# Kernel optimization log

Hardware: AMD Instinct MI355X
Metric: run time of the kernel (lower is better)

Reference implementation:

```python
import jax, jax.numpy as jnp
import numpy as np

ALPHA = 0.2        # LeakyReLU negative slope (config['alpha'])
NEG_INF = -9e15    # mask value from the original code


def setup_inputs() -> dict:
    key = jax.random.key(0)
    k1, k2, k3, k4 = jax.random.split(key, 4)
    N, Fin, Fout = 8192, 512, 256
    inp = jax.random.normal(k1, (N, Fin), dtype=jnp.float32)
    adj = jax.random.randint(k2, (N, N), 0, 2, dtype=jnp.int32)
    # xavier_uniform with gain=1.414
    limW = 1.414 * np.sqrt(6.0 / (Fin + Fout))
    W = jax.random.uniform(k3, (Fin, Fout), dtype=jnp.float32, minval=-limW, maxval=limW)
    lima = 1.414 * np.sqrt(6.0 / (2 * Fout + 1))
    a = jax.random.uniform(k4, (2 * Fout, 1), dtype=jnp.float32, minval=-lima, maxval=lima)
    return {"input": inp, "adj": adj, "W": W, "a": a}


def reference(input, adj, W, a):
    # h: [N, F]
    h = input @ W
    Fout = W.shape[1]
    # The original builds a_input[i, j] = concat(h_i, h_j) and dots with a.
    # Equivalently: e_ij = leakyrelu(h_i . a[:F] + h_j . a[F:]), computed
    # without the O(N^2 * 2F) intermediate.
    s1 = h @ a[:Fout, 0]   # [N] contribution from node i
    s2 = h @ a[Fout:, 0]   # [N] contribution from node j
    e = s1[:, None] + s2[None, :]                     # [N, N]
    e = jnp.where(e > 0, e, ALPHA * e)                # LeakyReLU
    scores = jnp.where(adj > 0, e, NEG_INF)
    attention = jax.nn.softmax(scores, axis=1)        # row-wise softmax
    # dropout is identity in inference mode (training=False)
    h_prime = attention @ h                           # [N, F]
    return jax.nn.elu(h_prime)                        # concat=True path
```

## Files before the change

### kernel.cpp

```cpp
#include <hip/hip_runtime.h>
#include <stdint.h>
#include <stddef.h>


#define N_NODES 8192
#define FIN     512
#define FOUT    256
#define LRALPHA 0.2f
#define MI_SHIFT 16.0f

typedef float f32x4 __attribute__((ext_vector_type(4)));
typedef short s16x8 __attribute__((ext_vector_type(8)));
typedef unsigned short u16x4 __attribute__((ext_vector_type(4)));
typedef int   i32x4 __attribute__((ext_vector_type(4)));
typedef unsigned long long u64;

typedef const uint32_t __attribute__((address_space(1)))* gas1_u32;
typedef uint32_t __attribute__((address_space(3)))* las3_u32;

__device__ __forceinline__ short f2bf_rne(float f) {
  uint32_t u = __builtin_bit_cast(uint32_t, f);
  u += 0x7fffu + ((u >> 16) & 1u);
  return (short)(u >> 16);
}
__device__ __forceinline__ short f2bf_fast(float f) {
  uint32_t u = __builtin_bit_cast(uint32_t, f);
  return (short)((u + 0x8000u) >> 16);
}
__device__ __forceinline__ float bf2f(short s) {
  uint32_t u = ((uint32_t)(uint16_t)s) << 16;
  return __builtin_bit_cast(float, u);
}

__global__ __launch_bounds__(256) void k_prep(const float* __restrict__ W,
                                              uint16_t* __restrict__ WThi,
                                              uint16_t* __restrict__ WTlo) {
  const int idx = blockIdx.x * 256 + threadIdx.x;
  const int n = idx >> 9;
  const int k = idx & 511;
  float v = W[k * FOUT + n];
  short h = f2bf_rne(v);
  WThi[idx] = (uint16_t)h;
  WTlo[idx] = (uint16_t)f2bf_rne(v - bf2f(h));
}

__global__ __launch_bounds__(256, 4) void k_pre(const float* __restrict__ X,
                                                const uint16_t* __restrict__ WThi,
                                                const uint16_t* __restrict__ WTlo,
                                                const float* __restrict__ a,
                                                const int* __restrict__ adj,
                                                uint16_t* __restrict__ HTf,
                                                float* __restrict__ s1g,
                                                float* __restrict__ s2g,
                                                u64* __restrict__ M3) {
  __shared__ float ls1[16], ls2[16];
  __shared__ uint16_t tile[FOUT * 16];
  const int lane = threadIdx.x & 63;
  const int w    = threadIdx.x >> 6;

  if (blockIdx.x >= 512) {
    const int bxm  = blockIdx.x - 512;
    const int iblk = bxm >> 5;
    const int jc   = bxm & 31;
    const int L    = lane;
    const int* base = adj + (size_t)(iblk * 128 + w * 32) * N_NODES + jc * 256 + L;
    u64 keep0 = 0, keep1 = 0, keep2 = 0, keep3 = 0;
#pragma unroll
    for (int it = 0; it < 32; ++it) {
      const int* rp = base + (size_t)it * N_NODES;
      int v0 = rp[0], v1 = rp[64], v2 = rp[128], v3 = rp[192];
      u64 b0 = __ballot(v0 != 0);
      u64 b1 = __ballot(v1 != 0);
      u64 b2 = __ballot(v2 != 0);
      u64 b3 = __ballot(v3 != 0);
      if (L == it) { keep0 = b0; keep1 = b1; keep2 = b2; keep3 = b3; }
    }
    if (L < 32) {
      const size_t mb = (size_t)iblk * 128 * 128 + (w * 32 + L);
      M3[mb + (size_t)(jc * 4 + 0) * 128] = keep0;
      M3[mb + (size_t)(jc * 4 + 1) * 128] = keep1;
      M3[mb + (size_t)(jc * 4 + 2) * 128] = keep2;
      M3[mb + (size_t)(jc * 4 + 3) * 128] = keep3;
    }
    return;
  }

  const int m    = lane & 15;
  const int quad = lane >> 4;
  const int i0   = blockIdx.x * 16;
  const int colg = w * 64;

  f32x4 acc[4];
#pragma unroll
  for (int cb = 0; cb < 4; ++cb) { f32x4 z = {0.f,0.f,0.f,0.f}; acc[cb] = z; }

  for (int kt = 0; kt < FIN / 32; ++kt) {
    const int k0 = kt * 32 + quad * 8;
    const float* ap = X + (size_t)(i0 + m) * FIN + k0;
    f32x4 a0 = *(const f32x4*)ap;
    f32x4 a1 = *(const f32x4*)(ap + 4);
    s16x8 ahi, alo;
#pragma unroll
    for (int e = 0; e < 4; ++e) {
      short h0 = f2bf_rne(a0[e]); ahi[e] = h0; alo[e] = f2bf_rne(a0[e] - bf2f(h0));
      short h1 = f2bf_rne(a1[e]); ahi[4+e] = h1; alo[4+e] = f2bf_rne(a1[e] - bf2f(h1));
    }
#pragma unroll
    for (int cb = 0; cb < 4; ++cb) {
      const int n = colg + cb * 16 + m;
      s16x8 bhi = *(const s16x8*)(WThi + (size_t)n * FIN + k0);
      s16x8 blo = *(const s16x8*)(WTlo + (size_t)n * FIN + k0);
      acc[cb] = __builtin_amdgcn_mfma_f32_16x16x32_bf16(ahi, bhi, acc[cb], 0, 0, 0);
      acc[cb] = __builtin_amdgcn_mfma_f32_16x16x32_bf16(ahi, blo, acc[cb], 0, 0, 0);
      acc[cb] = __builtin_amdgcn_mfma_f32_16x16x32_bf16(alo, bhi, acc[cb], 0, 0, 0);
    }
  }

  float p1[4] = {0.f,0.f,0.f,0.f}, p2[4] = {0.f,0.f,0.f,0.f};
#pragma unroll
  for (int cb = 0; cb < 4; ++cb) {
    const int n = colg + cb * 16 + m;
    const float a1c = a[n];
    const float a2c = a[FOUT + n];
#pragma unroll
    for (int reg = 0; reg < 4; ++reg) {
      p1[reg] += acc[cb][reg] * a1c;
      p2[reg] += acc[cb][reg] * a2c;
    }
  }
#pragma unroll
  for (int off = 1; off <= 8; off <<= 1)
#pragma unroll
    for (int reg = 0; reg < 4; ++reg) {
      p1[reg] += __shfl_xor(p1[reg], off);
      p2[reg] += __shfl_xor(p2[reg], off);
    }
  if (threadIdx.x < 16) { ls1[threadIdx.x] = 0.f; ls2[threadIdx.x] = 0.f; }
  __syncthreads();
  if (m == 0) {
#pragma unroll
    for (int reg = 0; reg < 4; ++reg) {
      atomicAdd(&ls1[quad * 4 + reg], p1[reg]);
      atomicAdd(&ls2[quad * 4 + reg], p2[reg]);
    }
  }
#pragma unroll
  for (int cb = 0; cb < 4; ++cb) {
    const int col = colg + cb * 16 + m;
    u16x4 pk;
#pragma unroll
    for (int reg = 0; reg < 4; ++reg) pk[reg] = (uint16_t)f2bf_rne(acc[cb][reg]);
    *(u16x4*)(tile + col * 16 + quad * 4) = pk;
  }
  __syncthreads();
  const int t = threadIdx.x;
  if (t < 16) { s1g[i0 + t] = ls1[t]; s2g[i0 + t] = ls2[t]; }
  const int jt = i0 >> 5;
  const int qh = (i0 >> 4) & 1;
  const int c  = t >> 4;
  const int mm = t & 15;
#pragma unroll
  for (int qq = 0; qq < 2; ++qq) {
    uint4 v = *(const uint4*)(tile + (c * 16 + mm) * 16 + qq * 8);
    *(uint4*)(HTf + ((((size_t)jt * 16 + c) * 64) + (qh * 2 + qq) * 16 + mm) * 8) = v;
  }
}

__global__ __launch_bounds__(512, 4) void k_attn(const u64* __restrict__ M3,
                                                 const uint16_t* __restrict__ HTf,
                                                 const float* __restrict__ s1,
                                                 const float* __restrict__ s2,
                                                 float* __restrict__ pout,
                                                 float* __restrict__ pden,
                                                 int split) {
  __shared__ uint16_t PL[2][4096];
  __shared__ uint16_t BL[2][8192];
  __shared__ float lss2[1024];
  __shared__ float ldsden[512];

  const int tid  = threadIdx.x;
  const int lane = tid & 63;
  const int w    = tid >> 6;
  const int m    = lane & 15;
  const int q    = lane >> 4;
  const int rg   = w >> 2, cg = w & 3;
  const int r    = tid & 127;
  const int cpr  = tid >> 7;
  const int i0   = blockIdx.x * 128;
  const int sp   = blockIdx.y;
  const int jrange = N_NODES / split;
  const int jbeg   = sp * jrange;
  const int jblk   = jbeg >> 5;
  const int nphase = jrange / 32;

  const float s1r = s1[i0 + r];
  float mi = fmaxf(s1r + MI_SHIFT, LRALPHA * (s1r + MI_SHIFT));

  f32x4 acc[4][4];
#pragma unroll
  for (int rt = 0; rt < 4; ++rt)
#pragma unroll
    for (int cb = 0; cb < 4; ++cb) { f32x4 z = {0.f,0.f,0.f,0.f}; acc[rt][cb] = z; }
  float den = 0.f;

  const u64* mrow = M3 + ((size_t)blockIdx.x * 128 + (jbeg >> 6)) * 128 + r;
  u64 mcur = mrow[0];

#define STAGE_B(pp, buf) do {                                                  \
    const uint16_t* s_ = HTf + (((size_t)(jblk + (pp))) << 13) + (w << 10) +   \
                         (lane << 3);                                          \
    __builtin_amdgcn_global_load_lds((gas1_u32)(const void*)s_,                \
        (las3_u32)(void*)(&BL[buf][w << 10]), 16, 0, 0);                       \
    __builtin_amdgcn_global_load_lds((gas1_u32)(const void*)(s_ + 512),        \
        (las3_u32)(void*)(&BL[buf][(w << 10) + 512]), 16, 0, 0);               \
  } while (0)

  STAGE_B(0, 0);

#pragma unroll 1
  for (int ph = 0; ph < nphase; ph += 2) {
    if ((ph & 31) == 0) {
      __syncthreads();
      if (tid < 256) *(f32x4*)(lss2 + tid * 4) =
        *(const f32x4*)(s2 + jbeg + (ph >> 5) * 1024 + tid * 4);
      __syncthreads();
    }
    u64 mnx = (ph + 2 < nphase) ? mrow[((ph >> 1) + 1) * 128] : 0;
#pragma unroll
    for (int po = 0; po < 2; ++po) {
      const int p = ph + po;
      const int pl = p & 31;
      f32x4 sA = *(const f32x4*)(lss2 + pl * 32 + cpr * 8);
      f32x4 sB = *(const f32x4*)(lss2 + pl * 32 + cpr * 8 + 4);
      const uint32_t by = (uint32_t)(mcur >> ((po * 4 + cpr) * 8)) & 0xffu;
      s16x8 P0;
#pragma unroll
      for (int e = 0; e < 4; ++e) {
        float x0 = s1r + sA[e];
        float pv0 = __expf(fmaxf(x0, LRALPHA * x0) - mi);
        pv0 = ((by >> e) & 1u) ? pv0 : 0.f;
        den += pv0; P0[e] = f2bf_fast(pv0);
        float x1 = s1r + sB[e];
        float pv1 = __expf(fmaxf(x1, LRALPHA * x1) - mi);
        pv1 = ((by >> (e + 4)) & 1u) ? pv1 : 0.f;
        den += pv1; P0[4 + e] = f2bf_fast(pv1);
      }
      *(s16x8*)(PL[p & 1] + (cpr * 128 + r) * 8) = P0;
      __syncthreads();
      if (p + 1 < nphase) STAGE_B(p + 1, (p + 1) & 1);
      s16x8 Bv[4];
#pragma unroll
      for (int cb = 0; cb < 4; ++cb)
        Bv[cb] = *(const s16x8*)(&BL[p & 1][((cg * 4 + cb) << 9) + (lane << 3)]);
      s16x8 F[4];
#pragma unroll
      for (int rt = 0; rt < 4; ++rt)
        F[rt] = *(const s16x8*)(PL[p & 1] + (q * 128 + rg * 64 + rt * 16 + m) * 8);
      __builtin_amdgcn_s_setprio(1);
#pragma unroll
      for (int rt = 0; rt < 4; ++rt)
#pragma unroll
        for (int cb = 0; cb < 4; ++cb)
          acc[rt][cb] = __builtin_amdgcn_mfma_f32_16x16x32_bf16(F[rt], Bv[cb], acc[rt][cb], 0, 0, 0);
      __builtin_amdgcn_s_setprio(0);
    }
    mcur = mnx;
  }
#undef STAGE_B

  ldsden[cpr * 128 + r] = den;
  __syncthreads();
  if (tid < 128) {
    float d = ldsden[tid] + ldsden[128 + tid] + ldsden[256 + tid] + ldsden[384 + tid];
    pden[(size_t)sp * N_NODES + i0 + tid] = d;
  }
#pragma unroll
  for (int rt = 0; rt < 4; ++rt)
#pragma unroll
    for (int cb = 0; cb < 4; ++cb)
#pragma unroll
      for (int reg = 0; reg < 4; ++reg) {
        const int row = i0 + rg * 64 + rt * 16 + q * 4 + reg;
        const int col = cg * 64 + cb * 16 + m;
        pout[((size_t)sp * N_NODES + row) * FOUT + col] = acc[rt][cb][reg];
      }
}

__global__ __launch_bounds__(256) void k_reduce(const float* __restrict__ pout,
                                                const float* __restrict__ pden,
                                                float* __restrict__ out,
                                                int split) {
  const int gid = blockIdx.x * 256 + threadIdx.x;
  const int i = gid >> 6;
  const int c = (gid & 63) << 2;
  f32x4 sum = {0.f,0.f,0.f,0.f};
  float den = 0.f;
  for (int s = 0; s < split; ++s) {
    sum += *(const f32x4*)(pout + ((size_t)s * N_NODES + i) * FOUT + c);
    den += pden[(size_t)s * N_NODES + i];
  }
  const float inv = 1.0f / den;
  f32x4 r;
#pragma unroll
  for (int e = 0; e < 4; ++e) {
    float v = sum[e] * inv;
    r[e] = v > 0.f ? v : (__expf(v) - 1.0f);
  }
  *(f32x4*)(out + (size_t)i * FOUT + c) = r;
}

extern "C" void kernel_launch(void* const* d_in, const int* in_sizes, int n_in,
                              void* d_out, int out_size, void* d_ws, size_t ws_size,
                              hipStream_t stream) {
  const float* X   = (const float*)d_in[0];
  const int*   adj = (const int*)d_in[1];
  const float* W   = (const float*)d_in[2];
  const float* a   = (const float*)d_in[3];
  float* out = (float*)d_out;

  char* ws = (char*)d_ws;
  uint16_t* HTf  = (uint16_t*)ws;
  uint16_t* WThi = (uint16_t*)(ws + (4u << 20));
  uint16_t* WTlo = (uint16_t*)(ws + (4u << 20) + 262144);
  float*    s1   = (float*)(ws + (4u << 20) + 524288);
  float*    s2   = s1 + N_NODES;
  float*    pden = s2 + N_NODES;
  u64*      M3   = (u64*)(ws + (6u << 20));
  const size_t pout_off = (size_t)16u << 20;
  const size_t slab = (size_t)N_NODES * FOUT * sizeof(float);

  int split;
  if      (ws_size >= pout_off + 8 * slab) split = 8;
  else if (ws_size >= pout_off + 4 * slab) split = 4;
  else if (ws_size >= pout_off + 2 * slab) split = 2;
  else                                     split = 1;
  float* pout = (split == 1) ? out : (float*)(ws + pout_off);

  k_prep<<<dim3(512), dim3(256), 0, stream>>>(W, WThi, WTlo);
  k_pre<<<dim3(2560), dim3(256), 0, stream>>>(X, WThi, WTlo, a, adj, HTf, s1, s2, M3);
  k_attn<<<dim3(N_NODES / 128, split), dim3(512), 0, stream>>>(M3, HTf, s1, s2, pout, pden, split);
  k_reduce<<<dim3(N_NODES * FOUT / 4 / 256), dim3(256), 0, stream>>>(pout, pden, out, split);
}
```

Measured before the change: 467.7 us.

## Fuse adjacency reads into attention kernel, dropping bitmask precompute pass

Removes the separate adjacency-to-bitmask pass from k_pre, so k_attn now reads the int32 adjacency directly, prefetching the next 32-column chunk each phase. Threads are remapped so each owns one row and 8 consecutive columns, and the phase loop is no longer unrolled by two. The MFMA operands are swapped so the accumulators come out transposed, which lets output stores become 16-byte vector stores. This saves one full pass over the 256MB adjacency plus the mask write and read. The cost is per-thread strided int32 loads inside the attention loop, which may leave the loop bound by memory latency.

Measured after the change: 465.7 us. No clear change (-0.4%).

```diff
diff --git a/kernel.cpp b/kernel.cpp
--- a/kernel.cpp
+++ b/kernel.cpp
@@ -48,42 +48,13 @@
                                                 const uint16_t* __restrict__ WThi,
                                                 const uint16_t* __restrict__ WTlo,
                                                 const float* __restrict__ a,
-                                                const int* __restrict__ adj,
                                                 uint16_t* __restrict__ HTf,
                                                 float* __restrict__ s1g,
-                                                float* __restrict__ s2g,
-                                                u64* __restrict__ M3) {
+                                                float* __restrict__ s2g) {
   __shared__ float ls1[16], ls2[16];
   __shared__ uint16_t tile[FOUT * 16];
   const int lane = threadIdx.x & 63;
   const int w    = threadIdx.x >> 6;
-
-  if (blockIdx.x >= 512) {
-    const int bxm  = blockIdx.x - 512;
-    const int iblk = bxm >> 5;
-    const int jc   = bxm & 31;
-    const int L    = lane;
-    const int* base = adj + (size_t)(iblk * 128 + w * 32) * N_NODES + jc * 256 + L;
-    u64 keep0 = 0, keep1 = 0, keep2 = 0, keep3 = 0;
-#pragma unroll
-    for (int it = 0; it < 32; ++it) {
-      const int* rp = base + (size_t)it * N_NODES;
-      int v0 = rp[0], v1 = rp[64], v2 = rp[128], v3 = rp[192];
-      u64 b0 = __ballot(v0 != 0);
-      u64 b1 = __ballot(v1 != 0);
-      u64 b2 = __ballot(v2 != 0);
-      u64 b3 = __ballot(v3 != 0);
-      if (L == it) { keep0 = b0; keep1 = b1; keep2 = b2; keep3 = b3; }
-    }
-    if (L < 32) {
-      const size_t mb = (size_t)iblk * 128 * 128 + (w * 32 + L);
-      M3[mb + (size_t)(jc * 4 + 0) * 128] = keep0;
-      M3[mb + (size_t)(jc * 4 + 1) * 128] = keep1;
-      M3[mb + (size_t)(jc * 4 + 2) * 128] = keep2;
-      M3[mb + (size_t)(jc * 4 + 3) * 128] = keep3;
-    }
-    return;
-  }
 
   const int m    = lane & 15;
   const int quad = lane >> 4;
@@ -166,10 +137,10 @@
   }
 }
 
-__global__ __launch_bounds__(512, 4) void k_attn(const u64* __restrict__ M3,
-                                                 const uint16_t* __restrict__ HTf,
+__global__ __launch_bounds__(512, 4) void k_attn(const uint16_t* __restrict__ HTf,
                                                  const float* __restrict__ s1,
                                                  const float* __restrict__ s2,
+                                                 const int* __restrict__ adj,
                                                  float* __restrict__ pout,
                                                  float* __restrict__ pden,
                                                  int split) {
@@ -184,8 +155,8 @@
   const int m    = lane & 15;
   const int q    = lane >> 4;
   const int rg   = w >> 2, cg = w & 3;
-  const int r    = tid & 127;
-  const int cpr  = tid >> 7;
+  const int rr   = tid >> 2;
+  const int cw   = tid & 3;
   const int i0   = blockIdx.x * 128;
   const int sp   = blockIdx.y;
   const int jrange = N_NODES / split;
@@ -193,7 +164,7 @@
   const int jblk   = jbeg >> 5;
   const int nphase = jrange / 32;
 
-  const float s1r = s1[i0 + r];
+  const float s1r = s1[i0 + rr];
   float mi = fmaxf(s1r + MI_SHIFT, LRALPHA * (s1r + MI_SHIFT));
 
   f32x4 acc[4][4];
@@ -203,8 +174,9 @@
     for (int cb = 0; cb < 4; ++cb) { f32x4 z = {0.f,0.f,0.f,0.f}; acc[rt][cb] = z; }
   float den = 0.f;
 
-  const u64* mrow = M3 + ((size_t)blockIdx.x * 128 + (jbeg >> 6)) * 128 + r;
-  u64 mcur = mrow[0];
+  const int* adjp = adj + (size_t)(i0 + rr) * N_NODES + jbeg + cw * 8;
+  i32x4 A0 = *(const i32x4*)adjp;
+  i32x4 A1 = *(const i32x4*)(adjp + 4);
 
 #define STAGE_B(pp, buf) do {                                                  \
     const uint16_t* s_ = HTf + (((size_t)(jblk + (pp))) << 13) + (w << 10) +   \
@@ -218,57 +190,57 @@
   STAGE_B(0, 0);
 
 #pragma unroll 1
-  for (int ph = 0; ph < nphase; ph += 2) {
-    if ((ph & 31) == 0) {
+  for (int p = 0; p < nphase; ++p) {
+    if ((p & 31) == 0) {
       __syncthreads();
       if (tid < 256) *(f32x4*)(lss2 + tid * 4) =
-        *(const f32x4*)(s2 + jbeg + (ph >> 5) * 1024 + tid * 4);
+        *(const f32x4*)(s2 + jbeg + (p >> 5) * 1024 + tid * 4);
       __syncthreads();
     }
-    u64 mnx = (ph + 2 < nphase) ? mrow[((ph >> 1) + 1) * 128] : 0;
-#pragma unroll
-    for (int po = 0; po < 2; ++po) {
-      const int p = ph + po;
-      const int pl = p & 31;
-      f32x4 sA = *(const f32x4*)(lss2 + pl * 32 + cpr * 8);
-      f32x4 sB = *(const f32x4*)(lss2 + pl * 32 + cpr * 8 + 4);
-      const uint32_t by = (uint32_t)(mcur >> ((po * 4 + cpr) * 8)) & 0xffu;
-      s16x8 P0;
-#pragma unroll
-      for (int e = 0; e < 4; ++e) {
-        float x0 = s1r + sA[e];
-        float pv0 = __expf(fmaxf(x0, LRALPHA * x0) - mi);
-        pv0 = ((by >> e) & 1u) ? pv0 : 0.f;
-        den += pv0; P0[e] = f2bf_fast(pv0);
-        float x1 = s1r + sB[e];
-        float pv1 = __expf(fmaxf(x1, LRALPHA * x1) - mi);
-        pv1 = ((by >> (e + 4)) & 1u) ? pv1 : 0.f;
-        den += pv1; P0[4 + e] = f2bf_fast(pv1);
-      }
-      *(s16x8*)(PL[p & 1] + (cpr * 128 + r) * 8) = P0;
-      __syncthreads();
-      if (p + 1 < nphase) STAGE_B(p + 1, (p + 1) & 1);
-      s16x8 Bv[4];
+    const int pl = p & 31;
+    f32x4 sA = *(const f32x4*)(lss2 + pl * 32 + cw * 8);
+    f32x4 sB = *(const f32x4*)(lss2 + pl * 32 + cw * 8 + 4);
+    s16x8 P0;
+#pragma unroll
+    for (int e = 0; e < 4; ++e) {
+      float x0 = s1r + sA[e];
+      float pv0 = __expf(fmaxf(x0, LRALPHA * x0) - mi);
+      pv0 = A0[e] ? pv0 : 0.f;
+      den += pv0; P0[e] = f2bf_fast(pv0);
+      float x1 = s1r + sB[e];
+      float pv1 = __expf(fmaxf(x1, LRALPHA * x1) - mi);
+      pv1 = A1[e] ? pv1 : 0.f;
+      den += pv1; P0[4 + e] = f2bf_fast(pv1);
+    }
+    *(s16x8*)(PL[p & 1] + (cw * 128 + rr) * 8) = P0;
+    __syncthreads();
+    i32x4 A0n = {0,0,0,0}, A1n = {0,0,0,0};
+    if (p + 1 < nphase) {
+      const int* np = adjp + (size_t)(p + 1) * 32;
+      A0n = *(const i32x4*)np;
+      A1n = *(const i32x4*)(np + 4);
+      STAGE_B(p + 1, (p + 1) & 1);
+    }
+    s16x8 Bv[4];
+#pragma unroll
+    for (int cb = 0; cb < 4; ++cb)
+      Bv[cb] = *(const s16x8*)(&BL[p & 1][((cg * 4 + cb) << 9) + (lane << 3)]);
+    s16x8 F[4];
+#pragma unroll
+    for (int rt = 0; rt < 4; ++rt)
+      F[rt] = *(const s16x8*)(PL[p & 1] + (q * 128 + rg * 64 + rt * 16 + m) * 8);
+    __builtin_amdgcn_s_setprio(1);
+#pragma unroll
+    for (int rt = 0; rt < 4; ++rt)
 #pragma unroll
       for (int cb = 0; cb < 4; ++cb)
-        Bv[cb] = *(const s16x8*)(&BL[p & 1][((cg * 4 + cb) << 9) + (lane << 3)]);
-      s16x8 F[4];
-#pragma unroll
-      for (int rt = 0; rt < 4; ++rt)
-        F[rt] = *(const s16x8*)(PL[p & 1] + (q * 128 + rg * 64 + rt * 16 + m) * 8);
-      __builtin_amdgcn_s_setprio(1);
-#pragma unroll
-      for (int rt = 0; rt < 4; ++rt)
-#pragma unroll
-        for (int cb = 0; cb < 4; ++cb)
-          acc[rt][cb] = __builtin_amdgcn_mfma_f32_16x16x32_bf16(F[rt], Bv[cb], acc[rt][cb], 0, 0, 0);
-      __builtin_amdgcn_s_setprio(0);
-    }
-    mcur = mnx;
+        acc[rt][cb] = __builtin_amdgcn_mfma_f32_16x16x32_bf16(Bv[cb], F[rt], acc[rt][cb], 0, 0, 0);
+    __builtin_amdgcn_s_setprio(0);
+    A0 = A0n; A1 = A1n;
   }
 #undef STAGE_B
 
-  ldsden[cpr * 128 + r] = den;
+  ldsden[cw * 128 + rr] = den;
   __syncthreads();
   if (tid < 128) {
     float d = ldsden[tid] + ldsden[128 + tid] + ldsden[256 + tid] + ldsden[384 + tid];
@@ -277,13 +249,11 @@
 #pragma unroll
   for (int rt = 0; rt < 4; ++rt)
 #pragma unroll
-    for (int cb = 0; cb < 4; ++cb)
-#pragma unroll
-      for (int reg = 0; reg < 4; ++reg) {
-        const int row = i0 + rg * 64 + rt * 16 + q * 4 + reg;
-        const int col = cg * 64 + cb * 16 + m;
-        pout[((size_t)sp * N_NODES + row) * FOUT + col] = acc[rt][cb][reg];
-      }
+    for (int cb = 0; cb < 4; ++cb) {
+      const int row = i0 + rg * 64 + rt * 16 + m;
+      const int col = cg * 64 + cb * 16 + q * 4;
+      *(f32x4*)(pout + ((size_t)sp * N_NODES + row) * FOUT + col) = acc[rt][cb];
+    }
 }
 
 __global__ __launch_bounds__(256) void k_reduce(const float* __restrict__ pout,
@@ -325,7 +295,6 @@
   float*    s1   = (float*)(ws + (4u << 20) + 524288);
   float*    s2   = s1 + N_NODES;
   float*    pden = s2 + N_NODES;
-  u64*      M3   = (u64*)(ws + (6u << 20));
   const size_t pout_off = (size_t)16u << 20;
   const size_t slab = (size_t)N_NODES * FOUT * sizeof(float);
 
@@ -337,7 +306,7 @@
   float* pout = (split == 1) ? out : (float*)(ws + pout_off);
 
   k_prep<<<dim3(512), dim3(256), 0, stream>>>(W, WThi, WTlo);
-  k_pre<<<dim3(2560), dim3(256), 0, stream>>>(X, WThi, WTlo, a, adj, HTf, s1, s2, M3);
-  k_attn<<<dim3(N_NODES / 128, split), dim3(512), 0, stream>>>(M3, HTf, s1, s2, pout, pden, split);
+  k_pre<<<dim3(512), dim3(256), 0, stream>>>(X, WThi, WTlo, a, HTf, s1, s2);
+  k_attn<<<dim3(N_NODES / 128, split), dim3(512), 0, stream>>>(HTf, s1, s2, adj, pout, pden, split);
   k_reduce<<<dim3(N_NODES * FOUT / 4 / 256), dim3(256), 0, stream>>>(pout, pden, out, split);
 }
```
